# Kernel tuning notes

Measured on AMD Instinct MI355X. Metric: run time of the kernel, lower is better.

The kernel has to match this reference:

```python
import jax, jax.numpy as jnp
import numpy as np

N, E, F, H, G = 50000, 800000, 64, 64, 100

def setup_inputs() -> dict:
    key = jax.random.key(0)
    ks = jax.random.split(key, 12)
    x = jax.random.normal(ks[0], (N, F), dtype=jnp.float32)
    edge_index = jax.random.randint(ks[1], (2, E), 0, N, dtype=jnp.int64)
    batch = jnp.sort(jax.random.randint(ks[2], (N,), 0, G, dtype=jnp.int64))
    s1 = 1.0 / np.sqrt(F); s2 = 1.0 / np.sqrt(H)
    W1 = jax.random.normal(ks[3], (2, F, H), dtype=jnp.float32) * s1
    b1 = jnp.zeros((H,), dtype=jnp.float32)
    W2 = jax.random.normal(ks[4], (2, H, H), dtype=jnp.float32) * s2
    b2 = jnp.zeros((H,), dtype=jnp.float32)
    gamma = jnp.ones((H,), dtype=jnp.float32)
    beta = jnp.zeros((H,), dtype=jnp.float32)
    linW = jax.random.normal(ks[5], (H, 1), dtype=jnp.float32) * s2
    linb = jnp.zeros((1,), dtype=jnp.float32)
    return {"x": x, "edge_index": edge_index, "batch": batch, "W1": W1, "b1": b1,
            "W2": W2, "b2": b2, "gamma": gamma, "beta": beta, "linW": linW, "linb": linb}

def _edge_norm(row, col, n):
    # get_laplacian(sym) + lambda_max=2: Lhat off-diag weight = -d_i^{-1/2} d_j^{-1/2}, diag = 0
    deg = jax.ops.segment_sum(jnp.ones(row.shape[0], jnp.float32), row, num_segments=n)
    dis = jnp.where(deg > 0, deg ** -0.5, 0.0)
    return -dis[row] * dis[col]

def _cheb(x, row, col, w, W, b):
    # K=2: out = T0(Lhat)x @ W0 + T1(Lhat)x @ W1 + b, T1 = Lhat x via scatter-add
    Tx1 = jax.ops.segment_sum(w[:, None] * x[row], col, num_segments=x.shape[0])
    return x @ W[0] + Tx1 @ W[1] + b

def reference(x, edge_index, batch, W1, b1, W2, b2, gamma, beta, linW, linb):
    row, col = edge_index[0], edge_index[1]
    n = x.shape[0]
    w = _edge_norm(row, col, n)
    h = _cheb(x, row, col, w, W1, b1)
    # BatchNorm1d (training-mode batch stats, eps=1e-5)
    mu = jnp.mean(h, axis=0)
    var = jnp.var(h, axis=0)
    h = (h - mu) * jax.lax.rsqrt(var + 1e-5) * gamma + beta
    # LeakyReLU (default slope 0.01)
    h = jnp.where(h >= 0, h, 0.01 * h)
    h = _cheb(h, row, col, w, W2, b2)
    # global_mean_pool over graph ids
    sums = jax.ops.segment_sum(h, batch, num_segments=G)
    cnts = jax.ops.segment_sum(jnp.ones(n, jnp.float32), batch, num_segments=G)
    pooled = sums / jnp.maximum(cnts, 1.0)[:, None]
    # dropout: identity (eval)
    return pooled @ linW + linb
```

## Files before the change

### kernel.cpp

```cpp
#include <hip/hip_runtime.h>

#define HDIM 64
#define BH 64
#define HNODES 25600
#define HBINS 12800
#define SBINS 12544
#define GR 32


__device__ __forceinline__ int lbound(const int* __restrict__ b, int n, int v) {
    int lo = 0, hi = n;
    while (lo < hi) { int m = (lo + hi) >> 1; if (b[m] < v) lo = m + 1; else hi = m; }
    return lo;
}

__device__ __forceinline__ unsigned short f2bf(float f) {
    unsigned u = __float_as_uint(f);
    unsigned r = u + 0x7FFFu + ((u >> 16) & 1u);
    return (unsigned short)(r >> 16);
}
__device__ __forceinline__ float bf2f(unsigned short s) {
    return __uint_as_float((unsigned)s << 16);
}


__global__ __launch_bounds__(256) void k_histP(const int* __restrict__ row,
                                               const int* __restrict__ col,
                                               unsigned short* __restrict__ cntP,
                                               unsigned short* __restrict__ degP,
                                               int E, int N, int slice) {
    __shared__ unsigned hbin[HBINS];
    int blk   = blockIdx.x;
    int phase = blockIdx.y & 1;
    int isRow = blockIdx.y >> 1;
    const int* keys = isRow ? row : col;
    unsigned short* outP = isRow ? degP : cntP;
    int lo = phase * HNODES;
    int spanN = min(HNODES, N - lo);
    int binsU = (spanN + 1) >> 1;
    for (int i = threadIdx.x; i < binsU; i += 256) hbin[i] = 0;
    __syncthreads();
    int e0 = blk * slice, e1 = min(e0 + slice, E);
    for (int e = e0 + threadIdx.x; e < e1; e += 256) {
        int c = keys[e] - lo;
        if ((unsigned)c < (unsigned)spanN)
            atomicAdd(&hbin[c >> 1], 1u << ((c & 1) << 4));
    }
    __syncthreads();
    unsigned* outU = (unsigned*)(outP + (size_t)blk * N + lo);
    for (int i = threadIdx.x; i < binsU; i += 256) outU[i] = hbin[i];
}

__global__ void k_prefA(unsigned short* __restrict__ cntP,
                        const unsigned short* __restrict__ degP,
                        int* __restrict__ cnt, float* __restrict__ dis, int N) {
    int i = blockIdx.x * blockDim.x + threadIdx.x;
    if (i >= N) return;
    int run = 0;
    #pragma unroll 8
    for (int b = 0; b < BH; ++b) {
        int v = cntP[(size_t)b * N + i];
        cntP[(size_t)b * N + i] = (unsigned short)run;
        run += v;
    }
    cnt[i] = run;
    int d = 0;
    #pragma unroll 8
    for (int b = 0; b < BH; ++b) d += degP[(size_t)b * N + i];
    dis[i] = d > 0 ? rsqrtf((float)d) : 0.0f;
}

__global__ __launch_bounds__(1024) void k_scan1(const int* __restrict__ cnt,
                                                int* __restrict__ start,
                                                int* __restrict__ bsum, int n) {
    __shared__ int wsum[16];
    int i = blockIdx.x * 1024 + threadIdx.x;
    int lane = threadIdx.x & 63, w = threadIdx.x >> 6;
    int v = (i < n) ? cnt[i] : 0;
    int incl = v;
    #pragma unroll
    for (int off = 1; off < 64; off <<= 1) {
        int u = __shfl_up(incl, off, 64);
        if (lane >= off) incl += u;
    }
    if (lane == 63) wsum[w] = incl;
    __syncthreads();
    if (w == 0) {
        int s = (lane < 16) ? wsum[lane] : 0;
        int si = s;
        #pragma unroll
        for (int off = 1; off < 16; off <<= 1) {
            int u = __shfl_up(si, off, 64);
            if (lane >= off) si += u;
        }
        if (lane < 16) wsum[lane] = si - s;
    }
    __syncthreads();
    int excl = incl - v + wsum[w];
    if (i < n) start[i] = excl;
    if (threadIdx.x == 1023) bsum[blockIdx.x] = excl + v;
}

__global__ void k_scan2(int* __restrict__ bsum, int nb) {
    int lane = threadIdx.x;
    if (lane >= 64) return;
    int v = (lane < nb) ? bsum[lane] : 0;
    int incl = v;
    #pragma unroll
    for (int off = 1; off < 64; off <<= 1) {
        int u = __shfl_up(incl, off, 64);
        if (lane >= off) incl += u;
    }
    if (lane < nb) bsum[lane] = incl - v;
}

__global__ void k_scan3(int* __restrict__ start, const int* __restrict__ bsum, int n) {
    int i = blockIdx.x * blockDim.x + threadIdx.x;
    if (i < n) start[i] += bsum[i >> 10];
}

__global__ __launch_bounds__(256) void k_sortfill(const int* __restrict__ row,
                                                  const int* __restrict__ col,
                                                  const unsigned short* __restrict__ cntP,
                                                  const int* __restrict__ start,
                                                  int* __restrict__ er,
                                                  int E, int N, int slice) {
    __shared__ int cur[SBINS];
    int blk = blockIdx.x;
    int lo = blockIdx.y * SBINS;
    int span = min(SBINS, N - lo);
    for (int i = threadIdx.x; i < span; i += 256)
        cur[i] = start[lo + i] + (int)cntP[(size_t)blk * N + lo + i];
    __syncthreads();
    int e0 = blk * slice, e1 = min(e0 + slice, E);
    for (int e = e0 + threadIdx.x; e < e1; e += 256) {
        int c = col[e] - lo;
        int rv = row[e];
        if ((unsigned)c < (unsigned)span) {
            int pos = atomicAdd(&cur[c], 1);
            er[pos] = rv;
        }
    }
}


__global__ __launch_bounds__(512) void k_gemm2(const float* __restrict__ x,
                                               const float* __restrict__ dis,
                                               const float* __restrict__ W1,
                                               const float* __restrict__ b1,
                                               float* __restrict__ z,
                                               unsigned short* __restrict__ y16, int n) {
    __shared__ float xs[GR][HDIM];
    int tid  = threadIdx.x;
    int j    = tid & 63;
    int half = (tid >> 6) & 1;
    int w2   = tid >> 7;
    int base = blockIdx.x * GR;

    const float* Wb = W1 + (half ? HDIM * HDIM : 0);
    float4 wr[16];
    #pragma unroll
    for (int k4 = 0; k4 < 16; ++k4) {
        wr[k4].x = Wb[(k4 * 4 + 0) * HDIM + j];
        wr[k4].y = Wb[(k4 * 4 + 1) * HDIM + j];
        wr[k4].z = Wb[(k4 * 4 + 2) * HDIM + j];
        wr[k4].w = Wb[(k4 * 4 + 3) * HDIM + j];
    }
    float bj = b1[j];

    {
        int v = tid;
        int r = base + (v >> 4);
        int rc = min(r, n - 1);
        int c = (v & 15) * 4;
        ((float4*)xs)[v] = *(const float4*)&x[(size_t)rc * HDIM + c];
    }
    __syncthreads();

    #pragma unroll
    for (int m = 0; m < 8; ++m) {
        int lr = w2 * 8 + m;
        int r = base + lr;
        if (r < n) {
            const float4* rp = (const float4*)xs[lr];
            float a = 0.f;
            #pragma unroll
            for (int k4 = 0; k4 < 16; ++k4) {
                float4 v = rp[k4];
                a = fmaf(v.x, wr[k4].x, a);
                a = fmaf(v.y, wr[k4].y, a);
                a = fmaf(v.z, wr[k4].z, a);
                a = fmaf(v.w, wr[k4].w, a);
            }
            if (half == 0) z[(size_t)r * HDIM + j] = a + bj;
            else           y16[(size_t)r * HDIM + j] = f2bf(dis[r] * a);
        }
    }
}

__global__ __launch_bounds__(256) void k_gatherH(const int* __restrict__ er,
                                                 const int* __restrict__ start,
                                                 const int* __restrict__ cnt,
                                                 const float* __restrict__ dis,
                                                 const unsigned short* __restrict__ y16,
                                                 const float* __restrict__ z,
                                                 float* __restrict__ h,
                                                 float* __restrict__ pstat, int n) {
    __shared__ float red[2][4][HDIM];
    int w = threadIdx.x >> 6;
    int j = threadIdx.x & 63;
    float sacc = 0.f, ssacc = 0.f;
    #pragma unroll
    for (int m = 0; m < 4; ++m) {
        int i = blockIdx.x * 16 + w * 4 + m;
        if (i < n) {
            int s = start[i], nd = cnt[i];
            float a0 = 0.f, a1 = 0.f, a2 = 0.f, a3 = 0.f;
            int k = 0;
            for (; k + 3 < nd; k += 4) {
                int r0 = er[s + k], r1 = er[s + k + 1];
                int r2 = er[s + k + 2], r3 = er[s + k + 3];
                a0 += bf2f(y16[(size_t)r0 * HDIM + j]);
                a1 += bf2f(y16[(size_t)r1 * HDIM + j]);
                a2 += bf2f(y16[(size_t)r2 * HDIM + j]);
                a3 += bf2f(y16[(size_t)r3 * HDIM + j]);
            }
            for (; k < nd; ++k) a0 += bf2f(y16[(size_t)er[s + k] * HDIM + j]);
            float hv = z[(size_t)i * HDIM + j] - dis[i] * ((a0 + a1) + (a2 + a3));
            h[(size_t)i * HDIM + j] = hv;
            sacc += hv;
            ssacc = fmaf(hv, hv, ssacc);
        }
    }
    red[0][w][j] = sacc;
    red[1][w][j] = ssacc;
    __syncthreads();
    if (w == 0) {
        float s  = red[0][0][j] + red[0][1][j] + red[0][2][j] + red[0][3][j];
        float ss = red[1][0][j] + red[1][1][j] + red[1][2][j] + red[1][3][j];
        pstat[(size_t)blockIdx.x * 128 + j]      = s;
        pstat[(size_t)blockIdx.x * 128 + 64 + j] = ss;
    }
}

__global__ __launch_bounds__(256) void k_statred(const float* __restrict__ pstat,
                                                 float* __restrict__ stats, int nb) {
    int idx = blockIdx.x;
    float s = 0.f;
    for (int b = threadIdx.x; b < nb; b += 256)
        s += pstat[(size_t)b * 128 + idx];
    __shared__ float red[256];
    red[threadIdx.x] = s;
    __syncthreads();
    for (int off = 128; off > 0; off >>= 1) {
        if (threadIdx.x < off) red[threadIdx.x] += red[threadIdx.x + off];
        __syncthreads();
    }
    if (threadIdx.x == 0) stats[idx] = red[0];
}

__global__ void k_prep(const float* __restrict__ stats,
                       const float* __restrict__ gamma, const float* __restrict__ beta,
                       const float* __restrict__ W2, const float* __restrict__ b2,
                       const float* __restrict__ linW, const float* __restrict__ linb,
                       float* __restrict__ scale, float* __restrict__ shift,
                       float* __restrict__ u0, float* __restrict__ u1,
                       float* __restrict__ c0, int n) {
    int k = threadIdx.x;
    if (k >= HDIM) return;
    float inv_n = 1.0f / (float)n;
    float mu  = stats[k] * inv_n;
    float var = stats[64 + k] * inv_n - mu * mu;
    float rs  = rsqrtf(var + 1e-5f);
    float sc  = rs * gamma[k];
    scale[k] = sc;
    shift[k] = beta[k] - mu * sc;
    float a0 = 0.f, a1 = 0.f;
    #pragma unroll 8
    for (int j = 0; j < HDIM; ++j) {
        float lw = linW[j];
        a0 = fmaf(W2[k * HDIM + j], lw, a0);
        a1 = fmaf(W2[HDIM * HDIM + k * HDIM + j], lw, a1);
    }
    u0[k] = a0;
    u1[k] = a1;
    if (k == 0) {
        float c = linb[0];
        for (int j = 0; j < HDIM; ++j) c = fmaf(b2[j], linW[j], c);
        c0[0] = c;
    }
}

__global__ __launch_bounds__(256) void k_node(const float* __restrict__ h,
                                              const float* __restrict__ scale,
                                              const float* __restrict__ shift,
                                              const float* __restrict__ u0,
                                              const float* __restrict__ u1,
                                              const float* __restrict__ dis,
                                              float* __restrict__ a, float* __restrict__ t,
                                              int n) {
    int i = blockIdx.x * 4 + (threadIdx.x >> 6);
    if (i >= n) return;
    int j = threadIdx.x & 63;
    float v = fmaf(h[(size_t)i * HDIM + j], scale[j], shift[j]);
    v = v >= 0.f ? v : 0.01f * v;
    float p0 = v * u0[j];
    float p1 = v * u1[j];
    #pragma unroll
    for (int off = 32; off > 0; off >>= 1) {
        p0 += __shfl_xor(p0, off, 64);
        p1 += __shfl_xor(p1, off, 64);
    }
    if (j == 0) { a[i] = p0; t[i] = dis[i] * p1; }
}

__global__ void k_gather2(const int* __restrict__ er, const int* __restrict__ start,
                          const int* __restrict__ cnt, const float* __restrict__ dis,
                          const float* __restrict__ t, const float* __restrict__ a,
                          float* __restrict__ s2, int n) {
    int i = blockIdx.x * blockDim.x + threadIdx.x;
    if (i >= n) return;
    int s = start[i], nd = cnt[i];
    float s0 = 0.f, s1 = 0.f, s2v = 0.f, s3 = 0.f;
    int k = 0;
    for (; k + 3 < nd; k += 4) {
        s0 += t[er[s + k]];
        s1 += t[er[s + k + 1]];
        s2v += t[er[s + k + 2]];
        s3 += t[er[s + k + 3]];
    }
    for (; k < nd; ++k) s0 += t[er[s + k]];
    s2[i] = a[i] - dis[i] * ((s0 + s1) + (s2v + s3));
}

__global__ __launch_bounds__(256) void k_pool2(const float* __restrict__ s2,
                                               const int* __restrict__ batch,
                                               const float* __restrict__ c0,
                                               const float* __restrict__ linb,
                                               float* __restrict__ out, int n) {
    int g = blockIdx.x;
    int lo = lbound(batch, n, g);
    int hi = lbound(batch, n, g + 1);
    float s = 0.f;
    for (int i = lo + threadIdx.x; i < hi; i += 256) s += s2[i];
    __shared__ float red[256];
    red[threadIdx.x] = s;
    __syncthreads();
    for (int off = 128; off > 0; off >>= 1) {
        if (threadIdx.x < off) red[threadIdx.x] += red[threadIdx.x + off];
        __syncthreads();
    }
    if (threadIdx.x == 0) {
        int cntg = hi - lo;
        out[g] = cntg > 0 ? red[0] / (float)cntg + c0[0] : linb[0];
    }
}


extern "C" void kernel_launch(void* const* d_in, const int* in_sizes, int n_in,
                              void* d_out, int out_size, void* d_ws, size_t ws_size,
                              hipStream_t stream) {
    const float* x     = (const float*)d_in[0];
    const int*   eidx  = (const int*)d_in[1];
    const int*   batch = (const int*)d_in[2];
    const float* W1    = (const float*)d_in[3];
    const float* b1    = (const float*)d_in[4];
    const float* W2    = (const float*)d_in[5];
    const float* b2    = (const float*)d_in[6];
    const float* gamma = (const float*)d_in[7];
    const float* beta  = (const float*)d_in[8];
    const float* linW  = (const float*)d_in[9];
    const float* linb  = (const float*)d_in[10];
    float* out = (float*)d_out;

    const int N = in_sizes[0] / HDIM;
    const int E = in_sizes[1] / 2;
    const int G = out_size;
    const int NB = (N + 1023) / 1024;
    const int slice = (E + BH - 1) / BH;
    const int NHB = (N + 15) / 16;

    const int* row = eidx;
    const int* col = eidx + E;

    char* wsb = (char*)d_ws;
    float* h    = (float*)wsb;               wsb += (size_t)N * HDIM * 4;
    unsigned short* cntP = (unsigned short*)h;
    unsigned short* degP = cntP + (size_t)BH * N;
    float* z    = (float*)wsb;               wsb += (size_t)N * HDIM * 4;
    unsigned short* y16 = (unsigned short*)wsb; wsb += (size_t)N * HDIM * 2;
    int*   cnt   = (int*)wsb;                wsb += (size_t)N * 4;
    int*   start = (int*)wsb;                wsb += (size_t)N * 4;
    int*   bsum  = (int*)wsb;                wsb += (size_t)NB * 4 + 64;
    int*   er    = (int*)wsb;                wsb += (size_t)E * 4;
    float* dis   = (float*)wsb;              wsb += (size_t)N * 4;
    float* a     = (float*)wsb;              wsb += (size_t)N * 4;
    float* t     = (float*)wsb;              wsb += (size_t)N * 4;
    float* s2    = (float*)wsb;              wsb += (size_t)N * 4;
    float* pstat = (float*)wsb;              wsb += (size_t)NHB * 128 * 4;
    float* stats = (float*)wsb;              wsb += 128 * 4;
    float* scale = (float*)wsb;              wsb += HDIM * 4;
    float* shift = (float*)wsb;              wsb += HDIM * 4;
    float* u0    = (float*)wsb;              wsb += HDIM * 4;
    float* u1    = (float*)wsb;              wsb += HDIM * 4;
    float* c0    = (float*)wsb;              wsb += 64;

    k_histP<<<dim3(BH, 4), 256, 0, stream>>>(row, col, cntP, degP, E, N, slice);
    k_prefA<<<(N + 255) / 256, 256, 0, stream>>>(cntP, degP, cnt, dis, N);
    k_scan1<<<NB, 1024, 0, stream>>>(cnt, start, bsum, N);
    k_scan2<<<1, 64, 0, stream>>>(bsum, NB);
    k_scan3<<<(N + 255) / 256, 256, 0, stream>>>(start, bsum, N);
    k_sortfill<<<dim3(BH, 4), 256, 0, stream>>>(row, col, cntP, start, er, E, N, slice);
    k_gemm2<<<(N + GR - 1) / GR, 512, 0, stream>>>(x, dis, W1, b1, z, y16, N);
    k_gatherH<<<NHB, 256, 0, stream>>>(er, start, cnt, dis, y16, z, h, pstat, N);
    k_statred<<<128, 256, 0, stream>>>(pstat, stats, NHB);
    k_prep<<<1, 64, 0, stream>>>(stats, gamma, beta, W2, b2, linW, linb,
                                 scale, shift, u0, u1, c0, N);
    k_node<<<(N + 3) / 4, 256, 0, stream>>>(h, scale, shift, u0, u1, dis, a, t, N);
    k_gather2<<<(N + 255) / 256, 256, 0, stream>>>(er, start, cnt, dis, t, a, s2, N);
    k_pool2<<<G, 256, 0, stream>>>(s2, batch, c0, linb, out, N);
}
```

Baseline: 179.0 us.

## Use 8-bit per-block histograms and paired-bf16 vector loads in neighbor gather

```diff
diff --git a/kernel.cpp b/kernel.cpp
--- a/kernel.cpp
+++ b/kernel.cpp
@@ -1,9 +1,8 @@
 #include <hip/hip_runtime.h>
 
 #define HDIM 64
-#define BH 64
-#define HNODES 25600
-#define HBINS 12800
+#define BH 128
+#define HB8 12800
 #define SBINS 12544
 #define GR 32
 
@@ -19,53 +18,45 @@
     unsigned r = u + 0x7FFFu + ((u >> 16) & 1u);
     return (unsigned short)(r >> 16);
 }
-__device__ __forceinline__ float bf2f(unsigned short s) {
-    return __uint_as_float((unsigned)s << 16);
-}
-
-
-__global__ __launch_bounds__(256) void k_histP(const int* __restrict__ row,
+
+
+__global__ __launch_bounds__(256) void k_hist8(const int* __restrict__ row,
                                                const int* __restrict__ col,
-                                               unsigned short* __restrict__ cntP,
-                                               unsigned short* __restrict__ degP,
+                                               unsigned char* __restrict__ cntP,
+                                               unsigned char* __restrict__ degP,
                                                int E, int N, int slice) {
-    __shared__ unsigned hbin[HBINS];
-    int blk   = blockIdx.x;
-    int phase = blockIdx.y & 1;
-    int isRow = blockIdx.y >> 1;
-    const int* keys = isRow ? row : col;
-    unsigned short* outP = isRow ? degP : cntP;
-    int lo = phase * HNODES;
-    int spanN = min(HNODES, N - lo);
-    int binsU = (spanN + 1) >> 1;
+    __shared__ unsigned hbin[HB8];
+    int blk = blockIdx.x;
+    const int* keys = blockIdx.y ? row : col;
+    unsigned char* outP = blockIdx.y ? degP : cntP;
+    int binsU = (N + 3) >> 2;
     for (int i = threadIdx.x; i < binsU; i += 256) hbin[i] = 0;
     __syncthreads();
     int e0 = blk * slice, e1 = min(e0 + slice, E);
     for (int e = e0 + threadIdx.x; e < e1; e += 256) {
-        int c = keys[e] - lo;
-        if ((unsigned)c < (unsigned)spanN)
-            atomicAdd(&hbin[c >> 1], 1u << ((c & 1) << 4));
-    }
-    __syncthreads();
-    unsigned* outU = (unsigned*)(outP + (size_t)blk * N + lo);
+        int c = keys[e];
+        atomicAdd(&hbin[c >> 2], 1u << ((c & 3) << 3));
+    }
+    __syncthreads();
+    unsigned* outU = (unsigned*)(outP + (size_t)blk * N);
     for (int i = threadIdx.x; i < binsU; i += 256) outU[i] = hbin[i];
 }
 
-__global__ void k_prefA(unsigned short* __restrict__ cntP,
-                        const unsigned short* __restrict__ degP,
+__global__ void k_prefA(unsigned char* __restrict__ cntP,
+                        const unsigned char* __restrict__ degP,
                         int* __restrict__ cnt, float* __restrict__ dis, int N) {
     int i = blockIdx.x * blockDim.x + threadIdx.x;
     if (i >= N) return;
     int run = 0;
-    #pragma unroll 8
+    #pragma unroll 4
     for (int b = 0; b < BH; ++b) {
         int v = cntP[(size_t)b * N + i];
-        cntP[(size_t)b * N + i] = (unsigned short)run;
+        cntP[(size_t)b * N + i] = (unsigned char)run;
         run += v;
     }
     cnt[i] = run;
     int d = 0;
-    #pragma unroll 8
+    #pragma unroll 4
     for (int b = 0; b < BH; ++b) d += degP[(size_t)b * N + i];
     dis[i] = d > 0 ? rsqrtf((float)d) : 0.0f;
 }
@@ -121,7 +112,7 @@
 
 __global__ __launch_bounds__(256) void k_sortfill(const int* __restrict__ row,
                                                   const int* __restrict__ col,
-                                                  const unsigned short* __restrict__ cntP,
+                                                  const unsigned char* __restrict__ cntP,
                                                   const int* __restrict__ start,
                                                   int* __restrict__ er,
                                                   int E, int N, int slice) {
@@ -202,40 +193,61 @@
                                                  const int* __restrict__ start,
                                                  const int* __restrict__ cnt,
                                                  const float* __restrict__ dis,
-                                                 const unsigned short* __restrict__ y16,
+                                                 const unsigned* __restrict__ y32,
                                                  const float* __restrict__ z,
                                                  float* __restrict__ h,
                                                  float* __restrict__ pstat, int n) {
     __shared__ float red[2][4][HDIM];
     int w = threadIdx.x >> 6;
-    int j = threadIdx.x & 63;
-    float sacc = 0.f, ssacc = 0.f;
+    int lane = threadIdx.x & 63;
+    int l  = lane & 31;
+    int hi = lane >> 5;
+    float sx = 0.f, sy = 0.f, qx = 0.f, qy = 0.f;
     #pragma unroll
     for (int m = 0; m < 4; ++m) {
         int i = blockIdx.x * 16 + w * 4 + m;
-        if (i < n) {
-            int s = start[i], nd = cnt[i];
-            float a0 = 0.f, a1 = 0.f, a2 = 0.f, a3 = 0.f;
-            int k = 0;
-            for (; k + 3 < nd; k += 4) {
-                int r0 = er[s + k], r1 = er[s + k + 1];
-                int r2 = er[s + k + 2], r3 = er[s + k + 3];
-                a0 += bf2f(y16[(size_t)r0 * HDIM + j]);
-                a1 += bf2f(y16[(size_t)r1 * HDIM + j]);
-                a2 += bf2f(y16[(size_t)r2 * HDIM + j]);
-                a3 += bf2f(y16[(size_t)r3 * HDIM + j]);
+        if (i >= n) continue;
+        int s = start[i], nd = cnt[i];
+        float a0x = 0.f, a0y = 0.f, a1x = 0.f, a1y = 0.f;
+        int k = 0;
+        for (; k + 3 < nd; k += 4) {
+            int r0 = er[s + k + hi];
+            int r1 = er[s + k + 2 + hi];
+            unsigned v0 = y32[(size_t)r0 * 32 + l];
+            unsigned v1 = y32[(size_t)r1 * 32 + l];
+            a0x += __uint_as_float(v0 << 16);
+            a0y += __uint_as_float(v0 & 0xFFFF0000u);
+            a1x += __uint_as_float(v1 << 16);
+            a1y += __uint_as_float(v1 & 0xFFFF0000u);
+        }
+        for (; k < nd; k += 2) {
+            int idx = k + hi;
+            if (idx < nd) {
+                unsigned v = y32[(size_t)er[s + idx] * 32 + l];
+                a0x += __uint_as_float(v << 16);
+                a0y += __uint_as_float(v & 0xFFFF0000u);
             }
-            for (; k < nd; ++k) a0 += bf2f(y16[(size_t)er[s + k] * HDIM + j]);
-            float hv = z[(size_t)i * HDIM + j] - dis[i] * ((a0 + a1) + (a2 + a3));
-            h[(size_t)i * HDIM + j] = hv;
-            sacc += hv;
-            ssacc = fmaf(hv, hv, ssacc);
-        }
-    }
-    red[0][w][j] = sacc;
-    red[1][w][j] = ssacc;
+        }
+        float ax = a0x + a1x, ay = a0y + a1y;
+        ax += __shfl_xor(ax, 32, 64);
+        ay += __shfl_xor(ay, 32, 64);
+        if (hi == 0) {
+            float di = dis[i];
+            float2 zv = *(const float2*)&z[(size_t)i * HDIM + 2 * l];
+            float h0 = zv.x - di * ax;
+            float h1 = zv.y - di * ay;
+            *(float2*)&h[(size_t)i * HDIM + 2 * l] = make_float2(h0, h1);
+            sx += h0; sy += h1;
+            qx = fmaf(h0, h0, qx); qy = fmaf(h1, h1, qy);
+        }
+    }
+    if (hi == 0) {
+        *(float2*)&red[0][w][2 * l] = make_float2(sx, sy);
+        *(float2*)&red[1][w][2 * l] = make_float2(qx, qy);
+    }
     __syncthreads();
     if (w == 0) {
+        int j = lane;
         float s  = red[0][0][j] + red[0][1][j] + red[0][2][j] + red[0][3][j];
         float ss = red[1][0][j] + red[1][1][j] + red[1][2][j] + red[1][3][j];
         pstat[(size_t)blockIdx.x * 128 + j]      = s;
@@ -385,8 +397,8 @@
 
     char* wsb = (char*)d_ws;
     float* h    = (float*)wsb;               wsb += (size_t)N * HDIM * 4;
-    unsigned short* cntP = (unsigned short*)h;
-    unsigned short* degP = cntP + (size_t)BH * N;
+    unsigned char* cntP = (unsigned char*)h;
+    unsigned char* degP = cntP + (size_t)BH * N;
     float* z    = (float*)wsb;               wsb += (size_t)N * HDIM * 4;
     unsigned short* y16 = (unsigned short*)wsb; wsb += (size_t)N * HDIM * 2;
     int*   cnt   = (int*)wsb;                wsb += (size_t)N * 4;
@@ -405,14 +417,15 @@
     float* u1    = (float*)wsb;              wsb += HDIM * 4;
     float* c0    = (float*)wsb;              wsb += 64;
 
-    k_histP<<<dim3(BH, 4), 256, 0, stream>>>(row, col, cntP, degP, E, N, slice);
+    k_hist8<<<dim3(BH, 2), 256, 0, stream>>>(row, col, cntP, degP, E, N, slice);
     k_prefA<<<(N + 255) / 256, 256, 0, stream>>>(cntP, degP, cnt, dis, N);
     k_scan1<<<NB, 1024, 0, stream>>>(cnt, start, bsum, N);
     k_scan2<<<1, 64, 0, stream>>>(bsum, NB);
     k_scan3<<<(N + 255) / 256, 256, 0, stream>>>(start, bsum, N);
     k_sortfill<<<dim3(BH, 4), 256, 0, stream>>>(row, col, cntP, start, er, E, N, slice);
     k_gemm2<<<(N + GR - 1) / GR, 512, 0, stream>>>(x, dis, W1, b1, z, y16, N);
-    k_gatherH<<<NHB, 256, 0, stream>>>(er, start, cnt, dis, y16, z, h, pstat, N);
+    k_gatherH<<<NHB, 256, 0, stream>>>(er, start, cnt, dis, (const unsigned*)y16, z,
+                                       h, pstat, N);
     k_statred<<<128, 256, 0, stream>>>(pstat, stats, NHB);
     k_prep<<<1, 64, 0, stream>>>(stats, gamma, beta, W2, b2, linW, linb,
                                  scale, shift, u0, u1, c0, N);
```

New measurement: 173.5 us. 1.03x faster.
